# Kernel tuning notes

Measured on AMD Instinct MI355X. Metric: run time of the kernel, lower is better.

The kernel has to match this reference:

```python
import jax, jax.numpy as jnp
import numpy as np

T, P, E, H = 256, 256, 300, 256   # seq, batch(paragraphs), embed, lstm_size
M, C = 50000, 16384               # pair occurrences / candidates per type
MT, CT = 50000, 16384             # triple occurrences / candidates


def setup_inputs() -> dict:
    key = jax.random.key(0)
    ks = jax.random.split(key, 32)
    f = lambda i, shape, s=0.05: jax.random.normal(ks[i], shape, dtype=jnp.float32) * s
    inp = {
        "x": jax.random.normal(ks[0], (T, P, E), dtype=jnp.float32),
        # BiLSTM params (pytorch gate order i,f,g,o; b = b_ih + b_hh)
        "wih_f": f(1, (4 * H, E)), "whh_f": f(2, (4 * H, H)), "b_f": f(3, (4 * H,)),
        "wih_b": f(4, (4 * H, E)), "whh_b": f(5, (4 * H, H)), "b_b": f(6, (4 * H,)),
        # per-pair-type (drug-gene, drug-variant, gene-variant) stacked params
        "pair_hW": f(7, (3, 4 * H, 2 * H)), "pair_hb": f(8, (3, 2 * H)),
        "pair_oW": f(9, (3, 2 * H)), "pair_ob": f(10, (3,)),
        "pair_backoff": f(11, (3, 2 * H)),
        "tri_hW": f(12, (6 * H, 2 * H)), "tri_hb": f(13, (2 * H,)),
        "tri_backoff": f(14, (2 * H,)),
        "all_hW": f(15, (8 * H, 2 * H)), "all_hb": f(16, (2 * H,)),
        "out_tW": f(17, (2 * H,)), "out_tb": f(18, ()),
        # flattened (t*P+p) indices of mention starts, per pair type
        "occ1": jax.random.randint(ks[19], (3, M), 0, T * P, dtype=jnp.int32),
        "occ2": jax.random.randint(ks[20], (3, M), 0, T * P, dtype=jnp.int32),
        "seg": jax.random.randint(ks[21], (3, M), 0, C, dtype=jnp.int32),
        "tri_occ1": jax.random.randint(ks[22], (MT,), 0, T * P, dtype=jnp.int32),
        "tri_occ2": jax.random.randint(ks[23], (MT,), 0, T * P, dtype=jnp.int32),
        "tri_occ3": jax.random.randint(ks[24], (MT,), 0, T * P, dtype=jnp.int32),
        "tri_seg": jax.random.randint(ks[25], (MT,), 0, CT, dtype=jnp.int32),
        # pair candidate index looked up for each triple after removing entity i
        "tri_pair_idx": jax.random.randint(ks[26], (CT, 3), 0, C, dtype=jnp.int32),
    }
    return inp


def _lstm_dir(x, wih, whh, b):
    """Unidirectional LSTM over leading time axis. x: [T, P, E] -> [T, P, H]."""
    Pb, Hh = x.shape[1], whh.shape[1]
    def step(carry, xt):
        h, c = carry
        g = xt @ wih.T + h @ whh.T + b               # [P, 4H]
        i, fgate, gg, o = jnp.split(g, 4, axis=-1)
        c = jax.nn.sigmoid(fgate) * c + jax.nn.sigmoid(i) * jnp.tanh(gg)
        h = jax.nn.sigmoid(o) * jnp.tanh(c)
        return (h, c), h
    init = (jnp.zeros((Pb, Hh), x.dtype), jnp.zeros((Pb, Hh), x.dtype))
    _, hs = jax.lax.scan(step, init, x)
    return hs


def _forward(x, wih_f, whh_f, b_f, wih_b, whh_b, b_b, pair_hW, pair_hb, pair_oW,
             pair_ob, pair_backoff, tri_hW, tri_hb, tri_backoff, all_hW, all_hb,
             out_tW, out_tb, occ1, occ2, seg, tri_occ1, tri_occ2, tri_occ3,
             tri_seg, tri_pair_idx):
    hf = _lstm_dir(x, wih_f, whh_f, b_f)
    hb = _lstm_dir(x[::-1], wih_b, whh_b, b_b)[::-1]
    embs = jnp.concatenate([hf, hb], axis=-1)        # [T, P, 2H]
    flat = embs.reshape(-1, embs.shape[-1])          # [T*P, 2H]

    pair_vecs, pair_logits = [], []
    for k in range(3):  # fixed set of entity-type pairs
        v = jnp.concatenate([flat[occ1[k]], flat[occ2[k]]], axis=-1)   # [M, 4H]
        reps = v @ pair_hW[k] + pair_hb[k]                             # [M, 2H]
        counts = jax.ops.segment_sum(jnp.ones((reps.shape[0],), reps.dtype),
                                     seg[k], num_segments=C)
        pooled = jax.ops.segment_max(reps, seg[k], num_segments=C)
        pooled = jnp.where(counts[:, None] > 0, pooled, pair_backoff[k])
        pv = jnp.tanh(pooled)                                          # [C, 2H]
        pair_vecs.append(pv)
        pair_logits.append(pv @ pair_oW[k] + pair_ob[k])               # [C]

    tv = jnp.concatenate([flat[tri_occ1], flat[tri_occ2], flat[tri_occ3]], axis=-1)
    treps = tv @ tri_hW + tri_hb                                       # [MT, 2H]
    tcounts = jax.ops.segment_sum(jnp.ones((treps.shape[0],), treps.dtype),
                                  tri_seg, num_segments=CT)
    tpooled = jax.ops.segment_max(treps, tri_seg, num_segments=CT)
    tpooled = jnp.where(tcounts[:, None] > 0, tpooled, tri_backoff)
    triple_vecs = jnp.tanh(tpooled)                                    # [CT, 2H]

    # remove drug -> (gene,variant)=type2; remove gene -> (drug,variant)=type1;
    # remove variant -> (drug,gene)=type0
    feats = jnp.concatenate([pair_vecs[2][tri_pair_idx[:, 0]],
                             pair_vecs[1][tri_pair_idx[:, 1]],
                             pair_vecs[0][tri_pair_idx[:, 2]],
                             triple_vecs], axis=1)                     # [CT, 8H]
    final = jax.nn.relu(feats @ all_hW + all_hb)
    triple_logits = final @ out_tW + out_tb                            # [CT]
    return (triple_logits, jnp.stack(pair_logits))                     # [CT], [3, C]


def reference(x, wih_f, whh_f, b_f, wih_b, whh_b, b_b, pair_hW, pair_hb, pair_oW,
              pair_ob, pair_backoff, tri_hW, tri_hb, tri_backoff, all_hW, all_hb,
              out_tW, out_tb, occ1, occ2, seg, tri_occ1, tri_occ2, tri_occ3,
              tri_seg, tri_pair_idx):
    return _forward(x, wih_f, whh_f, b_f, wih_b, whh_b, b_b, pair_hW, pair_hb,
                    pair_oW, pair_ob, pair_backoff, tri_hW, tri_hb, tri_backoff,
                    all_hW, all_hb, out_tW, out_tb, occ1, occ2, seg, tri_occ1,
                    tri_occ2, tri_occ3, tri_seg, tri_pair_idx)
```

## Files before the change

kernel.cpp:

```cpp
#include <hip/hip_runtime.h>
#include <hip/hip_bf16.h>

#define T_  256
#define P_  256
#define E_  300
#define H_  256
#define M_  50000
#define C_  16384
#define MT_ 50000
#define CT_ 16384
#define D2H 512
#define D4H 1024
#define KCH 128

#define OFF_FLAT  0ull
#define OFF_PPOOL (OFF_FLAT  + (size_t)T_*P_*D2H*2)
#define OFF_TPOOL (OFF_PPOOL + (size_t)3*C_*D2H*4)
#define OFF_H     (OFF_TPOOL + (size_t)C_*D2H*4)
#define OFF_C     (OFF_H     + (size_t)2*2*P_*H_*4)
#define OFF_CNT   (OFF_C     + (size_t)2*P_*H_*4)
#define OFF_PWT   (OFF_CNT   + (size_t)4*C_*4)
#define OFF_TWT   (OFF_PWT   + (size_t)3*D2H*D4H*2)
#define OFF_AWT   (OFF_TWT   + (size_t)D2H*1536*2)
#define WS_NEED   (OFF_AWT   + (size_t)D2H*2048*2)
#define ZERO_BYTES (OFF_PWT - OFF_PPOOL)

typedef __attribute__((ext_vector_type(8))) short short8;
typedef __attribute__((ext_vector_type(4))) float floatx4;

__device__ __forceinline__ float bf2f(unsigned short u) {
    return __uint_as_float(((unsigned)u) << 16);
}
__device__ __forceinline__ unsigned short f2bf_rne(float f) {
    unsigned u = __float_as_uint(f);
    unsigned r = u + 0x7FFFu + ((u >> 16) & 1u);
    return (unsigned short)(r >> 16);
}
__device__ __forceinline__ unsigned fmap(float f) {
    unsigned u = __float_as_uint(f);
    return (u & 0x80000000u) ? ~u : (u | 0x80000000u);
}
__device__ __forceinline__ float funmap(unsigned k) {
    return __uint_as_float((k & 0x80000000u) ? (k ^ 0x80000000u) : ~k);
}
__device__ __forceinline__ float sigmoidf_(float x) { return 1.f / (1.f + __expf(-x)); }

__global__ __launch_bounds__(256) void transpose_bf16_kernel(
    const float* __restrict__ src, unsigned short* __restrict__ dst, int K, int N)
{
    __shared__ float tile[32][33];
    const int n0 = blockIdx.x << 5;
    const int k0 = blockIdx.y << 5;
    const int tx = threadIdx.x & 31;
    const int ty = threadIdx.x >> 5;
    #pragma unroll
    for (int i = 0; i < 4; ++i)
        tile[ty + (i << 3)][tx] = src[(size_t)(k0 + ty + (i << 3)) * N + n0 + tx];
    __syncthreads();
    #pragma unroll
    for (int i = 0; i < 4; ++i)
        dst[(size_t)(n0 + ty + (i << 3)) * K + k0 + tx] = f2bf_rne(tile[tx][ty + (i << 3)]);
}

__global__ __launch_bounds__(256) void lstm_step_kernel(
    const float* __restrict__ x,
    const float* __restrict__ wih_f, const float* __restrict__ whh_f, const float* __restrict__ b_f,
    const float* __restrict__ wih_b, const float* __restrict__ whh_b, const float* __restrict__ b_b,
    float* __restrict__ h_buf, float* __restrict__ c_buf,
    __hip_bfloat16* __restrict__ flat, int s)
{
    const int tid = threadIdx.x;
    const int bx  = blockIdx.x;
    const int dir = bx >> 7;
    const int rem = bx & 127;
    const int p0  = (rem >> 3) << 4;
    const int j0  = (rem & 7) << 5;
    const int t   = dir ? (T_ - 1 - s) : s;

    const float* wih = dir ? wih_b : wih_f;
    const float* whh = dir ? whh_b : whh_f;
    const float* bb  = dir ? b_b   : b_f;

    const int jj  = tid & 31;
    const int pg  = tid >> 5;
    const int pr0 = pg << 1;

    float acc[2][4] = {{0.f,0.f,0.f,0.f},{0.f,0.f,0.f,0.f}};

    __shared__ float As[16][33];
    __shared__ float Ws[32][128];

    const float* xt = x + (size_t)t * (P_ * E_);
    for (int kt = 0; kt < 10; ++kt) {
        const int kbase = kt << 5;
        {
            const int lp = tid >> 4;
            const int lk = (tid & 15) << 1;
            #pragma unroll
            for (int i = 0; i < 2; ++i) {
                const int k = kbase + lk + i;
                As[lp][lk + i] = (k < E_) ? xt[(size_t)(p0 + lp) * E_ + k] : 0.f;
            }
        }
        {
            const int col  = tid >> 1;
            const int grow = ((col >> 5) * H_) + j0 + (col & 31);
            const int lk0  = (tid & 1) << 4;
            const float* wrow = wih + (size_t)grow * E_;
            #pragma unroll
            for (int i = 0; i < 16; ++i) {
                const int k = kbase + lk0 + i;
                Ws[lk0 + i][col] = (k < E_) ? wrow[k] : 0.f;
            }
        }
        __syncthreads();
        #pragma unroll
        for (int kk = 0; kk < 32; ++kk) {
            const float a0 = As[pr0][kk], a1 = As[pr0 + 1][kk];
            const float w0 = Ws[kk][jj],      w1 = Ws[kk][jj + 32];
            const float w2 = Ws[kk][jj + 64], w3 = Ws[kk][jj + 96];
            acc[0][0] = fmaf(a0, w0, acc[0][0]); acc[0][1] = fmaf(a0, w1, acc[0][1]);
            acc[0][2] = fmaf(a0, w2, acc[0][2]); acc[0][3] = fmaf(a0, w3, acc[0][3]);
            acc[1][0] = fmaf(a1, w0, acc[1][0]); acc[1][1] = fmaf(a1, w1, acc[1][1]);
            acc[1][2] = fmaf(a1, w2, acc[1][2]); acc[1][3] = fmaf(a1, w3, acc[1][3]);
        }
        __syncthreads();
    }

    const float* hprev = h_buf + (size_t)((s & 1) * 2 + dir) * (P_ * H_);
    for (int kt = 0; kt < 8; ++kt) {
        const int kbase = kt << 5;
        {
            const int lp = tid >> 4;
            const int lk = (tid & 15) << 1;
            #pragma unroll
            for (int i = 0; i < 2; ++i)
                As[lp][lk + i] = hprev[(size_t)(p0 + lp) * H_ + kbase + lk + i];
        }
        {
            const int col  = tid >> 1;
            const int grow = ((col >> 5) * H_) + j0 + (col & 31);
            const int lk0  = (tid & 1) << 4;
            const float* wrow = whh + (size_t)grow * H_;
            #pragma unroll
            for (int i = 0; i < 16; ++i)
                Ws[lk0 + i][col] = wrow[kbase + lk0 + i];
        }
        __syncthreads();
        #pragma unroll
        for (int kk = 0; kk < 32; ++kk) {
            const float a0 = As[pr0][kk], a1 = As[pr0 + 1][kk];
            const float w0 = Ws[kk][jj],      w1 = Ws[kk][jj + 32];
            const float w2 = Ws[kk][jj + 64], w3 = Ws[kk][jj + 96];
            acc[0][0] = fmaf(a0, w0, acc[0][0]); acc[0][1] = fmaf(a0, w1, acc[0][1]);
            acc[0][2] = fmaf(a0, w2, acc[0][2]); acc[0][3] = fmaf(a0, w3, acc[0][3]);
            acc[1][0] = fmaf(a1, w0, acc[1][0]); acc[1][1] = fmaf(a1, w1, acc[1][1]);
            acc[1][2] = fmaf(a1, w2, acc[1][2]); acc[1][3] = fmaf(a1, w3, acc[1][3]);
        }
        __syncthreads();
    }

    const int j = j0 + jj;
    const float bi = bb[j], bfv = bb[H_ + j], bgv = bb[2 * H_ + j], bo = bb[3 * H_ + j];
    float* hnew = h_buf + (size_t)(((s & 1) ^ 1) * 2 + dir) * (P_ * H_);
    float* cst  = c_buf + (size_t)dir * (P_ * H_);
    #pragma unroll
    for (int i = 0; i < 2; ++i) {
        const int p = p0 + pr0 + i;
        const float gi = acc[i][0] + bi;
        const float gf = acc[i][1] + bfv;
        const float gg = acc[i][2] + bgv;
        const float go = acc[i][3] + bo;
        const size_t off = (size_t)p * H_ + j;
        const float cold = cst[off];
        const float cn = sigmoidf_(gf) * cold + sigmoidf_(gi) * tanhf(gg);
        const float hn = sigmoidf_(go) * tanhf(cn);
        cst[off]  = cn;
        hnew[off] = hn;
        flat[((size_t)t * P_ + p) * D2H + dir * H_ + j] = __float2bfloat16(hn);
    }
}

__global__ __launch_bounds__(256) void pair_mfma_kernel(
    const unsigned short* __restrict__ flat,
    const unsigned short* __restrict__ Wt,
    const float* __restrict__ hb,
    const int* __restrict__ occ1, const int* __restrict__ occ2,
    const int* __restrict__ seg,
    unsigned* __restrict__ pooled)
{
    const int type = blockIdx.z;
    const int m0 = blockIdx.x << 5;
    const int tid = threadIdx.x;
    const int wave = tid >> 6, lane = tid & 63;
    const int n0w = wave << 7;
    const int lrow = lane & 15, lk = lane >> 4;

    const unsigned short* W = Wt + (size_t)type * D2H * D4H;

    __shared__ unsigned short At[32][KCH + 8];

    floatx4 acc[2][8] = {};

    const int srow = tid >> 3;
    const int scol = (tid & 7) << 4;
    const int r = m0 + srow;
    const bool rv = (r < M_);
    const int i1 = rv ? occ1[type * M_ + r] : 0;
    const int i2 = rv ? occ2[type * M_ + r] : 0;

    for (int kc = 0; kc < D4H / KCH; ++kc) {
        {
            const int kg  = kc * KCH + scol;
            const int src = (kg < 512) ? i1 : i2;
            const int col = kg & 511;
            const unsigned short* p = flat + (size_t)src * D2H + col;
            *(uint4*)&At[srow][scol]     = *(const uint4*)p;
            *(uint4*)&At[srow][scol + 8] = *(const uint4*)(p + 8);
        }
        __syncthreads();
        #pragma unroll
        for (int ks = 0; ks < KCH / 32; ++ks) {
            short8 af0 = *(const short8*)&At[lrow]     [(ks << 5) + (lk << 3)];
            short8 af1 = *(const short8*)&At[16 + lrow][(ks << 5) + (lk << 3)];
            const int kgb = kc * KCH + (ks << 5) + (lk << 3);
            const unsigned short* wb = W + (size_t)(n0w + lrow) * D4H + kgb;
            #pragma unroll
            for (int f = 0; f < 8; ++f) {
                short8 bf = *(const short8*)(wb + (size_t)(f << 4) * D4H);
                acc[0][f] = __builtin_amdgcn_mfma_f32_16x16x32_bf16(af0, bf, acc[0][f], 0, 0, 0);
                acc[1][f] = __builtin_amdgcn_mfma_f32_16x16x32_bf16(af1, bf, acc[1][f], 0, 0, 0);
            }
        }
        __syncthreads();
    }

    int   segs[2][4];
    #pragma unroll
    for (int i = 0; i < 2; ++i)
        #pragma unroll
        for (int q = 0; q < 4; ++q) {
            const int row = m0 + (i << 4) + (lk << 2) + q;
            segs[i][q] = (row < M_) ? seg[type * M_ + row] : -1;
        }
    #pragma unroll
    for (int f = 0; f < 8; ++f) {
        const int col = n0w + (f << 4) + lrow;
        const float bias = hb[type * D2H + col];
        #pragma unroll
        for (int i = 0; i < 2; ++i)
            #pragma unroll
            for (int q = 0; q < 4; ++q) {
                if (segs[i][q] < 0) continue;
                atomicMax(pooled + ((size_t)type * C_ + segs[i][q]) * D2H + col,
                          fmap(acc[i][f][q] + bias));
            }
    }
}

__global__ __launch_bounds__(256) void tri_mfma_kernel(
    const unsigned short* __restrict__ flat,
    const unsigned short* __restrict__ Wt,
    const float* __restrict__ hb,
    const int* __restrict__ o1, const int* __restrict__ o2, const int* __restrict__ o3,
    const int* __restrict__ seg,
    unsigned* __restrict__ pooled)
{
    const int m0 = blockIdx.x << 5;
    const int tid = threadIdx.x;
    const int wave = tid >> 6, lane = tid & 63;
    const int n0w = wave << 7;
    const int lrow = lane & 15, lk = lane >> 4;
    const int K = 1536;

    __shared__ unsigned short At[32][KCH + 8];
    floatx4 acc[2][8] = {};

    const int srow = tid >> 3;
    const int scol = (tid & 7) << 4;
    const int r = m0 + srow;
    const bool rv = (r < MT_);
    const int i1 = rv ? o1[r] : 0;
    const int i2 = rv ? o2[r] : 0;
    const int i3 = rv ? o3[r] : 0;

    for (int kc = 0; kc < 12; ++kc) {
        {
            const int kg  = kc * KCH + scol;
            const int src = (kg < 512) ? i1 : (kg < 1024 ? i2 : i3);
            const int col = kg & 511;
            const unsigned short* p = flat + (size_t)src * D2H + col;
            *(uint4*)&At[srow][scol]     = *(const uint4*)p;
            *(uint4*)&At[srow][scol + 8] = *(const uint4*)(p + 8);
        }
        __syncthreads();
        #pragma unroll
        for (int ks = 0; ks < KCH / 32; ++ks) {
            short8 af0 = *(const short8*)&At[lrow]     [(ks << 5) + (lk << 3)];
            short8 af1 = *(const short8*)&At[16 + lrow][(ks << 5) + (lk << 3)];
            const int kgb = kc * KCH + (ks << 5) + (lk << 3);
            const unsigned short* wb = Wt + (size_t)(n0w + lrow) * K + kgb;
            #pragma unroll
            for (int f = 0; f < 8; ++f) {
                short8 bf = *(const short8*)(wb + (size_t)(f << 4) * K);
                acc[0][f] = __builtin_amdgcn_mfma_f32_16x16x32_bf16(af0, bf, acc[0][f], 0, 0, 0);
                acc[1][f] = __builtin_amdgcn_mfma_f32_16x16x32_bf16(af1, bf, acc[1][f], 0, 0, 0);
            }
        }
        __syncthreads();
    }

    int segs[2][4];
    #pragma unroll
    for (int i = 0; i < 2; ++i)
        #pragma unroll
        for (int q = 0; q < 4; ++q) {
            const int row = m0 + (i << 4) + (lk << 2) + q;
            segs[i][q] = (row < MT_) ? seg[row] : -1;
        }
    #pragma unroll
    for (int f = 0; f < 8; ++f) {
        const int col = n0w + (f << 4) + lrow;
        const float bias = hb[col];
        #pragma unroll
        for (int i = 0; i < 2; ++i)
            #pragma unroll
            for (int q = 0; q < 4; ++q) {
                if (segs[i][q] < 0) continue;
                atomicMax(pooled + (size_t)segs[i][q] * D2H + col,
                          fmap(acc[i][f][q] + bias));
            }
    }
}

__global__ void counts_kernel(const int* __restrict__ seg, const int* __restrict__ tri_seg,
                              int* __restrict__ counts)
{
    const int i = blockIdx.x * 256 + threadIdx.x;
    if (i < 3 * M_) {
        atomicAdd(&counts[(i / M_) * C_ + seg[i]], 1);
    } else {
        const int m = i - 3 * M_;
        if (m < MT_) atomicAdd(&counts[3 * C_ + tri_seg[m]], 1);
    }
}

__global__ __launch_bounds__(256) void pair_finalize_kernel(
    unsigned* __restrict__ pooled, const int* __restrict__ counts,
    const float* __restrict__ backoff, const float* __restrict__ oW,
    const float* __restrict__ ob, float* __restrict__ out)
{
    const int lane = threadIdx.x & 63;
    const int idx  = (blockIdx.x << 2) + (threadIdx.x >> 6);
    const int type = idx / C_;
    unsigned* row = pooled + (size_t)idx * D2H;
    const int cnt = counts[idx];
    float sum = 0.f;
    #pragma unroll
    for (int q = 0; q < 8; ++q) {
        const int col = (q << 6) + lane;
        const float v = (cnt > 0) ? funmap(row[col]) : backoff[type * D2H + col];
        const float pvv = tanhf(v);
        ((float*)row)[col] = pvv;
        sum += pvv * oW[type * D2H + col];
    }
    #pragma unroll
    for (int off = 32; off > 0; off >>= 1) sum += __shfl_down(sum, off);
    if (lane == 0) out[CT_ + idx] = sum + ob[type];
}

__global__ void tri_finalize_kernel(unsigned* __restrict__ tpool,
                                    const int* __restrict__ counts,
                                    const float* __restrict__ tri_backoff)
{
    const int gid = blockIdx.x * 256 + threadIdx.x;
    const int c = gid >> 9, col = gid & 511;
    const float v = (counts[3 * C_ + c] > 0) ? funmap(tpool[gid]) : tri_backoff[col];
    ((float*)tpool)[gid] = tanhf(v);
}

__global__ __launch_bounds__(256) void final_mfma_kernel(
    const float* __restrict__ pv,
    const float* __restrict__ trv,
    const unsigned short* __restrict__ Wt,
    const float* __restrict__ all_hb,
    const float* __restrict__ out_tW, const float* __restrict__ out_tb,
    const int* __restrict__ tpi,
    float* __restrict__ out)
{
    const int m0 = blockIdx.x << 5;
    const int tid = threadIdx.x;
    const int wave = tid >> 6, lane = tid & 63;
    const int n0w = wave << 7;
    const int lrow = lane & 15, lk = lane >> 4;
    const int K = 2048;

    __shared__ unsigned short At[32][KCH + 8];
    __shared__ float wpart[4][32];
    floatx4 acc[2][8] = {};

    const int srow = tid >> 3;
    const int scol = (tid & 7) << 4;
    const int r = m0 + srow;
    const float* srcs[4];
    srcs[0] = pv  + ((size_t)2 * C_ + tpi[r * 3 + 0]) * D2H;
    srcs[1] = pv  + ((size_t)1 * C_ + tpi[r * 3 + 1]) * D2H;
    srcs[2] = pv  + ((size_t)0 * C_ + tpi[r * 3 + 2]) * D2H;
    srcs[3] = trv + (size_t)r * D2H;

    for (int kc = 0; kc < 16; ++kc) {
        {
            const int kg  = kc * KCH + scol;
            const float* p = srcs[kg >> 9] + (kg & 511);
            unsigned short tmp[16];
            #pragma unroll
            for (int v4 = 0; v4 < 4; ++v4) {
                const float4 fv = *(const float4*)(p + (v4 << 2));
                tmp[v4 * 4 + 0] = f2bf_rne(fv.x);
                tmp[v4 * 4 + 1] = f2bf_rne(fv.y);
                tmp[v4 * 4 + 2] = f2bf_rne(fv.z);
                tmp[v4 * 4 + 3] = f2bf_rne(fv.w);
            }
            *(uint4*)&At[srow][scol]     = *(const uint4*)&tmp[0];
            *(uint4*)&At[srow][scol + 8] = *(const uint4*)&tmp[8];
        }
        __syncthreads();
        #pragma unroll
        for (int ks = 0; ks < KCH / 32; ++ks) {
            short8 af0 = *(const short8*)&At[lrow]     [(ks << 5) + (lk << 3)];
            short8 af1 = *(const short8*)&At[16 + lrow][(ks << 5) + (lk << 3)];
            const int kgb = kc * KCH + (ks << 5) + (lk << 3);
            const unsigned short* wb = Wt + (size_t)(n0w + lrow) * K + kgb;
            #pragma unroll
            for (int f = 0; f < 8; ++f) {
                short8 bf = *(const short8*)(wb + (size_t)(f << 4) * K);
                acc[0][f] = __builtin_amdgcn_mfma_f32_16x16x32_bf16(af0, bf, acc[0][f], 0, 0, 0);
                acc[1][f] = __builtin_amdgcn_mfma_f32_16x16x32_bf16(af1, bf, acc[1][f], 0, 0, 0);
            }
        }
        __syncthreads();
    }

    float psum[2][4] = {{0,0,0,0},{0,0,0,0}};
    #pragma unroll
    for (int f = 0; f < 8; ++f) {
        const int col = n0w + (f << 4) + lrow;
        const float bias = all_hb[col];
        const float w = out_tW[col];
        #pragma unroll
        for (int i = 0; i < 2; ++i)
            #pragma unroll
            for (int q = 0; q < 4; ++q)
                psum[i][q] = fmaf(fmaxf(acc[i][f][q] + bias, 0.f), w, psum[i][q]);
    }
    #pragma unroll
    for (int i = 0; i < 2; ++i)
        #pragma unroll
        for (int q = 0; q < 4; ++q) {
            float s = psum[i][q];
            s += __shfl_xor(s, 1); s += __shfl_xor(s, 2);
            s += __shfl_xor(s, 4); s += __shfl_xor(s, 8);
            if (lrow == 0) wpart[wave][(i << 4) + (lk << 2) + q] = s;
        }
    __syncthreads();
    if (tid < 32)
        out[m0 + tid] = wpart[0][tid] + wpart[1][tid] + wpart[2][tid] + wpart[3][tid]
                        + out_tb[0];
}

extern "C" void kernel_launch(void* const* d_in, const int* in_sizes, int n_in,
                              void* d_out, int out_size, void* d_ws, size_t ws_size,
                              hipStream_t stream)
{
    const float* x        = (const float*)d_in[0];
    const float* wih_f    = (const float*)d_in[1];
    const float* whh_f    = (const float*)d_in[2];
    const float* b_f      = (const float*)d_in[3];
    const float* wih_b    = (const float*)d_in[4];
    const float* whh_b    = (const float*)d_in[5];
    const float* b_b      = (const float*)d_in[6];
    const float* pair_hW  = (const float*)d_in[7];
    const float* pair_hb  = (const float*)d_in[8];
    const float* pair_oW  = (const float*)d_in[9];
    const float* pair_ob  = (const float*)d_in[10];
    const float* pair_bo  = (const float*)d_in[11];
    const float* tri_hW   = (const float*)d_in[12];
    const float* tri_hb   = (const float*)d_in[13];
    const float* tri_bo   = (const float*)d_in[14];
    const float* all_hW   = (const float*)d_in[15];
    const float* all_hb   = (const float*)d_in[16];
    const float* out_tW   = (const float*)d_in[17];
    const float* out_tb   = (const float*)d_in[18];
    const int*   occ1     = (const int*)d_in[19];
    const int*   occ2     = (const int*)d_in[20];
    const int*   seg      = (const int*)d_in[21];
    const int*   tri_occ1 = (const int*)d_in[22];
    const int*   tri_occ2 = (const int*)d_in[23];
    const int*   tri_occ3 = (const int*)d_in[24];
    const int*   tri_seg  = (const int*)d_in[25];
    const int*   tpi      = (const int*)d_in[26];

    if (ws_size < WS_NEED) return;

    char* ws = (char*)d_ws;
    __hip_bfloat16* flat = (__hip_bfloat16*)(ws + OFF_FLAT);
    unsigned* ppool      = (unsigned*)(ws + OFF_PPOOL);
    unsigned* tpool      = (unsigned*)(ws + OFF_TPOOL);
    float*    h_buf      = (float*)(ws + OFF_H);
    float*    c_buf      = (float*)(ws + OFF_C);
    int*      counts     = (int*)(ws + OFF_CNT);
    unsigned short* pwt  = (unsigned short*)(ws + OFF_PWT);
    unsigned short* twt  = (unsigned short*)(ws + OFF_TWT);
    unsigned short* awt  = (unsigned short*)(ws + OFF_AWT);
    float*    out        = (float*)d_out;

    hipMemsetAsync(ws + OFF_PPOOL, 0, ZERO_BYTES, stream);

    for (int t = 0; t < 3; ++t)
        transpose_bf16_kernel<<<dim3(D2H / 32, D4H / 32), 256, 0, stream>>>(
            pair_hW + (size_t)t * D4H * D2H, pwt + (size_t)t * D2H * D4H, D4H, D2H);
    transpose_bf16_kernel<<<dim3(D2H / 32, 1536 / 32), 256, 0, stream>>>(tri_hW, twt, 1536, D2H);
    transpose_bf16_kernel<<<dim3(D2H / 32, 2048 / 32), 256, 0, stream>>>(all_hW, awt, 2048, D2H);

    for (int s = 0; s < T_; ++s)
        lstm_step_kernel<<<256, 256, 0, stream>>>(x, wih_f, whh_f, b_f,
                                                  wih_b, whh_b, b_b,
                                                  h_buf, c_buf, flat, s);

    pair_mfma_kernel<<<dim3((M_ + 31) / 32, 1, 3), 256, 0, stream>>>(
        (const unsigned short*)flat, pwt, pair_hb, occ1, occ2, seg, ppool);
    tri_mfma_kernel<<<dim3((MT_ + 31) / 32), 256, 0, stream>>>(
        (const unsigned short*)flat, twt, tri_hb, tri_occ1, tri_occ2, tri_occ3, tri_seg, tpool);
    counts_kernel<<<(3 * M_ + MT_ + 255) / 256, 256, 0, stream>>>(seg, tri_seg, counts);

    pair_finalize_kernel<<<(3 * C_) / 4, 256, 0, stream>>>(
        ppool, counts, pair_bo, pair_oW, pair_ob, out);
    tri_finalize_kernel<<<(CT_ * D2H) / 256, 256, 0, stream>>>(tpool, counts, tri_bo);

    final_mfma_kernel<<<CT_ / 32, 256, 0, stream>>>(
        (const float*)ppool, (const float*)tpool, awt, all_hb, out_tW, out_tb, tpi, out);
}
```

Baseline: 9.028 ms.

## Hoist LSTM input projection into one MFMA GEMM and run persistent recurrence kernel

```diff
diff --git a/kernel.cpp b/kernel.cpp
--- a/kernel.cpp
+++ b/kernel.cpp
@@ -12,18 +12,24 @@
 #define D2H 512
 #define D4H 1024
 #define KCH 128
+#define KXW 320
 
 #define OFF_FLAT  0ull
-#define OFF_PPOOL (OFF_FLAT  + (size_t)T_*P_*D2H*2)
-#define OFF_TPOOL (OFF_PPOOL + (size_t)3*C_*D2H*4)
-#define OFF_H     (OFF_TPOOL + (size_t)C_*D2H*4)
+#define OFF_PWT   (OFF_FLAT  + (size_t)T_*P_*D2H*2)
+#define OFF_TWT   (OFF_PWT   + (size_t)3*D2H*D4H*2)
+#define OFF_AWT   (OFF_TWT   + (size_t)D2H*1536*2)
+#define OFF_WIHT  (OFF_AWT   + (size_t)D2H*2048*2)
+#define OFF_WHHB  (OFF_WIHT  + (size_t)2048*KXW*2)
+#define OFF_H     (OFF_WHHB  + (size_t)2048*H_*2)
 #define OFF_C     (OFF_H     + (size_t)2*2*P_*H_*4)
 #define OFF_CNT   (OFF_C     + (size_t)2*P_*H_*4)
-#define OFF_PWT   (OFF_CNT   + (size_t)4*C_*4)
-#define OFF_TWT   (OFF_PWT   + (size_t)3*D2H*D4H*2)
-#define OFF_AWT   (OFF_TWT   + (size_t)D2H*1536*2)
-#define WS_NEED   (OFF_AWT   + (size_t)D2H*2048*2)
-#define ZERO_BYTES (OFF_PWT - OFF_PPOOL)
+#define OFF_PPOOL (OFF_CNT   + (size_t)4*C_*4)
+#define OFF_TPOOL (OFF_PPOOL + (size_t)3*C_*D2H*4)
+#define WS_OLD    (OFF_TPOOL + (size_t)C_*D2H*4)
+#define OFF_XW    OFF_PPOOL
+#define WS_NEW    (OFF_XW    + (size_t)T_*P_*2048*2)
+#define ZERO_OFF  OFF_H
+#define ZERO_BYTES (WS_OLD - OFF_H)
 
 typedef __attribute__((ext_vector_type(8))) short short8;
 typedef __attribute__((ext_vector_type(4))) float floatx4;
@@ -60,6 +66,171 @@
     #pragma unroll
     for (int i = 0; i < 4; ++i)
         dst[(size_t)(n0 + ty + (i << 3)) * K + k0 + tx] = f2bf_rne(tile[tx][ty + (i << 3)]);
+}
+
+__global__ __launch_bounds__(320) void wih_cast_kernel(
+    const float* __restrict__ wih_f, const float* __restrict__ wih_b,
+    unsigned short* __restrict__ dst)
+{
+    const int n = blockIdx.x;
+    const int k = threadIdx.x;
+    float v = 0.f;
+    if (k < E_) v = (n < D4H) ? wih_f[(size_t)n * E_ + k]
+                              : wih_b[(size_t)(n - D4H) * E_ + k];
+    dst[(size_t)n * KXW + k] = f2bf_rne(v);
+}
+
+__global__ __launch_bounds__(256) void whh_cast_kernel(
+    const float* __restrict__ whh_f, const float* __restrict__ whh_b,
+    unsigned short* __restrict__ dst)
+{
+    const int n = blockIdx.x;
+    const int k = threadIdx.x;
+    const float v = (n < D4H) ? whh_f[(size_t)n * H_ + k]
+                              : whh_b[(size_t)(n - D4H) * H_ + k];
+    dst[(size_t)n * H_ + k] = f2bf_rne(v);
+}
+
+__global__ __launch_bounds__(256) void xw_gemm_kernel(
+    const float* __restrict__ x, const unsigned short* __restrict__ wihT,
+    const float* __restrict__ b_f, const float* __restrict__ b_b,
+    unsigned short* __restrict__ xw)
+{
+    const int m0 = blockIdx.x << 5;
+    const int tid = threadIdx.x;
+    const int wave = tid >> 6, lane = tid & 63;
+    const int n0w = (blockIdx.y << 9) + (wave << 7);
+    const int lrow = lane & 15, lk = lane >> 4;
+
+    __shared__ unsigned short At[32][KXW];
+
+    {
+        const int row = tid >> 3;
+        const int c0  = (tid & 7) * 40;
+        unsigned short tmp[40];
+        #pragma unroll
+        for (int i = 0; i < 10; ++i) {
+            const int c = c0 + (i << 2);
+            float4 v = {0.f, 0.f, 0.f, 0.f};
+            if (c < E_) v = *(const float4*)&x[(size_t)(m0 + row) * E_ + c];
+            tmp[(i << 2) + 0] = f2bf_rne(v.x);
+            tmp[(i << 2) + 1] = f2bf_rne(v.y);
+            tmp[(i << 2) + 2] = f2bf_rne(v.z);
+            tmp[(i << 2) + 3] = f2bf_rne(v.w);
+        }
+        #pragma unroll
+        for (int i = 0; i < 5; ++i)
+            *(uint4*)&At[row][c0 + (i << 3)] = *(const uint4*)&tmp[i << 3];
+    }
+    __syncthreads();
+
+    floatx4 acc[2][8] = {};
+    for (int kc = 0; kc < KXW / 32; ++kc) {
+        short8 af0 = *(const short8*)&At[lrow]     [(kc << 5) + (lk << 3)];
+        short8 af1 = *(const short8*)&At[16 + lrow][(kc << 5) + (lk << 3)];
+        const unsigned short* wb = wihT + (size_t)(n0w + lrow) * KXW + (kc << 5) + (lk << 3);
+        #pragma unroll
+        for (int f = 0; f < 8; ++f) {
+            short8 bf = *(const short8*)(wb + (size_t)(f << 4) * KXW);
+            acc[0][f] = __builtin_amdgcn_mfma_f32_16x16x32_bf16(af0, bf, acc[0][f], 0, 0, 0);
+            acc[1][f] = __builtin_amdgcn_mfma_f32_16x16x32_bf16(af1, bf, acc[1][f], 0, 0, 0);
+        }
+    }
+
+    #pragma unroll
+    for (int f = 0; f < 8; ++f) {
+        const int col = n0w + (f << 4) + lrow;
+        const float bias = (col < D4H) ? b_f[col] : b_b[col - D4H];
+        #pragma unroll
+        for (int i = 0; i < 2; ++i)
+            #pragma unroll
+            for (int q = 0; q < 4; ++q) {
+                const int row = m0 + (i << 4) + (lk << 2) + q;
+                xw[(size_t)row * 2048 + col] = f2bf_rne(acc[i][f][q] + bias);
+            }
+    }
+}
+
+__global__ __launch_bounds__(256) void lstm_recur_kernel(
+    const unsigned short* __restrict__ xw,
+    const unsigned short* __restrict__ whhT,
+    __hip_bfloat16* __restrict__ flat)
+{
+    const int bx  = blockIdx.x;
+    const int dir = bx & 1;
+    const int p0  = (bx >> 1) << 5;
+    const int tid = threadIdx.x;
+    const int wave = tid >> 6, lane = tid & 63;
+    const int lrow = lane & 15, lk = lane >> 4;
+
+    __shared__ unsigned short h_lds[2][32][H_];
+    __shared__ unsigned short xw_lds[32][D4H];
+
+    const unsigned short* whh = whhT + (size_t)dir * D4H * H_;
+
+    for (int i = tid; i < 2 * 32 * H_; i += 256) ((unsigned short*)h_lds)[i] = 0;
+
+    float cc[32];
+    #pragma unroll
+    for (int i = 0; i < 32; ++i) cc[i] = 0.f;
+    __syncthreads();
+
+    int cur = 0;
+    for (int s = 0; s < T_; ++s) {
+        const int t = dir ? (T_ - 1 - s) : s;
+
+        {
+            const unsigned short* src = xw + ((size_t)t * P_ + p0) * 2048 + dir * D4H;
+            #pragma unroll
+            for (int i = 0; i < 16; ++i) {
+                const int idx = tid + (i << 8);
+                const int row = idx >> 7;
+                const int cu  = (idx & 127) << 3;
+                *(uint4*)&xw_lds[row][cu] = *(const uint4*)(src + (size_t)row * 2048 + cu);
+            }
+        }
+
+        floatx4 acc[2][4][4] = {};
+        for (int kc = 0; kc < 8; ++kc) {
+            short8 af0 = *(const short8*)&h_lds[cur][lrow]     [(kc << 5) + (lk << 3)];
+            short8 af1 = *(const short8*)&h_lds[cur][16 + lrow][(kc << 5) + (lk << 3)];
+            #pragma unroll
+            for (int g = 0; g < 4; ++g)
+                #pragma unroll
+                for (int jt = 0; jt < 4; ++jt) {
+                    const int nrow = (g << 8) + (wave << 6) + (jt << 4) + lrow;
+                    short8 bf = *(const short8*)(whh + (size_t)nrow * H_ + (kc << 5) + (lk << 3));
+                    acc[0][g][jt] = __builtin_amdgcn_mfma_f32_16x16x32_bf16(af0, bf, acc[0][g][jt], 0, 0, 0);
+                    acc[1][g][jt] = __builtin_amdgcn_mfma_f32_16x16x32_bf16(af1, bf, acc[1][g][jt], 0, 0, 0);
+                }
+        }
+        __syncthreads();
+
+        const int nxt = cur ^ 1;
+        #pragma unroll
+        for (int mi = 0; mi < 2; ++mi)
+            #pragma unroll
+            for (int jt = 0; jt < 4; ++jt)
+                #pragma unroll
+                for (int q = 0; q < 4; ++q) {
+                    const int j    = (wave << 6) + (jt << 4) + lrow;
+                    const int ploc = (mi << 4) + (lk << 2) + q;
+                    const float gi = acc[mi][0][jt][q] + bf2f(xw_lds[ploc][j]);
+                    const float gf = acc[mi][1][jt][q] + bf2f(xw_lds[ploc][256 + j]);
+                    const float gg = acc[mi][2][jt][q] + bf2f(xw_lds[ploc][512 + j]);
+                    const float go = acc[mi][3][jt][q] + bf2f(xw_lds[ploc][768 + j]);
+                    const int ci = (mi << 4) + (jt << 2) + q;
+                    const float cn = sigmoidf_(gf) * cc[ci] + sigmoidf_(gi) * tanhf(gg);
+                    cc[ci] = cn;
+                    const float hn = sigmoidf_(go) * tanhf(cn);
+                    const unsigned short hb16 = f2bf_rne(hn);
+                    h_lds[nxt][ploc][j] = hb16;
+                    flat[((size_t)t * P_ + p0 + ploc) * D2H + dir * H_ + j] =
+                        *(const __hip_bfloat16*)&hb16;
+                }
+        __syncthreads();
+        cur = nxt;
+    }
 }
 
 __global__ __launch_bounds__(256) void lstm_step_kernel(
@@ -95,11 +266,11 @@
         const int kbase = kt << 5;
         {
             const int lp = tid >> 4;
-            const int lk = (tid & 15) << 1;
+            const int lkx = (tid & 15) << 1;
             #pragma unroll
             for (int i = 0; i < 2; ++i) {
-                const int k = kbase + lk + i;
-                As[lp][lk + i] = (k < E_) ? xt[(size_t)(p0 + lp) * E_ + k] : 0.f;
+                const int k = kbase + lkx + i;
+                As[lp][lkx + i] = (k < E_) ? xt[(size_t)(p0 + lp) * E_ + k] : 0.f;
             }
         }
         {
@@ -132,10 +303,10 @@
         const int kbase = kt << 5;
         {
             const int lp = tid >> 4;
-            const int lk = (tid & 15) << 1;
+            const int lkx = (tid & 15) << 1;
             #pragma unroll
             for (int i = 0; i < 2; ++i)
-                As[lp][lk + i] = hprev[(size_t)(p0 + lp) * H_ + kbase + lk + i];
+                As[lp][lkx + i] = hprev[(size_t)(p0 + lp) * H_ + kbase + lkx + i];
         }
         {
             const int col  = tid >> 1;
@@ -199,7 +370,6 @@
     const unsigned short* W = Wt + (size_t)type * D2H * D4H;
 
     __shared__ unsigned short At[32][KCH + 8];
-
     floatx4 acc[2][8] = {};
 
     const int srow = tid >> 3;
@@ -235,7 +405,7 @@
         __syncthreads();
     }
 
-    int   segs[2][4];
+    int segs[2][4];
     #pragma unroll
     for (int i = 0; i < 2; ++i)
         #pragma unroll
@@ -500,21 +670,24 @@
     const int*   tri_seg  = (const int*)d_in[25];
     const int*   tpi      = (const int*)d_in[26];
 
-    if (ws_size < WS_NEED) return;
+    if (ws_size < WS_OLD) return;
 
     char* ws = (char*)d_ws;
     __hip_bfloat16* flat = (__hip_bfloat16*)(ws + OFF_FLAT);
-    unsigned* ppool      = (unsigned*)(ws + OFF_PPOOL);
-    unsigned* tpool      = (unsigned*)(ws + OFF_TPOOL);
+    unsigned short* pwt  = (unsigned short*)(ws + OFF_PWT);
+    unsigned short* twt  = (unsigned short*)(ws + OFF_TWT);
+    unsigned short* awt  = (unsigned short*)(ws + OFF_AWT);
+    unsigned short* wihT = (unsigned short*)(ws + OFF_WIHT);
+    unsigned short* whhB = (unsigned short*)(ws + OFF_WHHB);
     float*    h_buf      = (float*)(ws + OFF_H);
     float*    c_buf      = (float*)(ws + OFF_C);
     int*      counts     = (int*)(ws + OFF_CNT);
-    unsigned short* pwt  = (unsigned short*)(ws + OFF_PWT);
-    unsigned short* twt  = (unsigned short*)(ws + OFF_TWT);
-    unsigned short* awt  = (unsigned short*)(ws + OFF_AWT);
+    unsigned* ppool      = (unsigned*)(ws + OFF_PPOOL);
+    unsigned* tpool      = (unsigned*)(ws + OFF_TPOOL);
+    unsigned short* xw   = (unsigned short*)(ws + OFF_XW);
     float*    out        = (float*)d_out;
 
-    hipMemsetAsync(ws + OFF_PPOOL, 0, ZERO_BYTES, stream);
+    const bool fast = (ws_size >= WS_NEW);
 
     for (int t = 0; t < 3; ++t)
         transpose_bf16_kernel<<<dim3(D2H / 32, D4H / 32), 256, 0, stream>>>(
@@ -522,10 +695,19 @@
     transpose_bf16_kernel<<<dim3(D2H / 32, 1536 / 32), 256, 0, stream>>>(tri_hW, twt, 1536, D2H);
     transpose_bf16_kernel<<<dim3(D2H / 32, 2048 / 32), 256, 0, stream>>>(all_hW, awt, 2048, D2H);
 
-    for (int s = 0; s < T_; ++s)
-        lstm_step_kernel<<<256, 256, 0, stream>>>(x, wih_f, whh_f, b_f,
-                                                  wih_b, whh_b, b_b,
-                                                  h_buf, c_buf, flat, s);
+    if (fast) {
+        wih_cast_kernel<<<2048, 320, 0, stream>>>(wih_f, wih_b, wihT);
+        whh_cast_kernel<<<2048, 256, 0, stream>>>(whh_f, whh_b, whhB);
+        xw_gemm_kernel<<<dim3(T_ * P_ / 32, 4), 256, 0, stream>>>(x, wihT, b_f, b_b, xw);
+        lstm_recur_kernel<<<16, 256, 0, stream>>>(xw, whhB, flat);
+        hipMemsetAsync(ws + ZERO_OFF, 0, ZERO_BYTES, stream);
+    } else {
+        hipMemsetAsync(ws + ZERO_OFF, 0, ZERO_BYTES, stream);
+        for (int s = 0; s < T_; ++s)
+            lstm_step_kernel<<<256, 256, 0, stream>>>(x, wih_f, whh_f, b_f,
+                                                      wih_b, whh_b, b_b,
+                                                      h_buf, c_buf, flat, s);
+    }
 
     pair_mfma_kernel<<<dim3((M_ + 31) / 32, 1, 3), 256, 0, stream>>>(
         (const unsigned short*)flat, pwt, pair_hb, occ1, occ2, seg, ppool);
```

Result: no change. 9.057 ms (+0.3%).
